# Kernel optimization log

Hardware: AMD Instinct MI355X
Metric: run time of the kernel (lower is better)

The kernel has to match this reference:

```python
import jax, jax.numpy as jnp
import numpy as np

N_EMBD = 256  # scale uses input channel dim C, per original code


def setup_inputs() -> dict:
    key = jax.random.key(0)
    k1, k2, k3, k4 = jax.random.split(key, 4)
    B, T, C, H = 512, 256, 256, 64
    x = jax.random.normal(k1, (B, T, C), dtype=jnp.float32)
    Wq = jax.random.normal(k2, (C, H), dtype=jnp.float32) * (C ** -0.5)
    Wk = jax.random.normal(k3, (C, H), dtype=jnp.float32) * (C ** -0.5)
    Wv = jax.random.normal(k4, (C, H), dtype=jnp.float32) * (C ** -0.5)
    return {"x": x, "Wq": Wq, "Wk": Wk, "Wv": Wv}


def reference(x, Wq, Wk, Wv):
    B, T, C = x.shape
    q = jnp.einsum("btc,ch->bth", x, Wq)  # [B,T,H]
    k = jnp.einsum("btc,ch->bth", x, Wk)
    v = jnp.einsum("btc,ch->bth", x, Wv)
    # Note: original scales by C**-0.5 (input dim), not head_size**-0.5.
    scores = jnp.einsum("bqh,bkh->bqk", q, k) * (C ** -0.5)  # [B,T,T]
    causal = jnp.tril(jnp.ones((T, T), dtype=bool))
    scores = jnp.where(causal, scores, -jnp.inf)
    weights = jax.nn.softmax(scores, axis=-1)
    # Dropout is identity at inference (Keras default training=False).
    out = jnp.einsum("bqk,bkh->bqh", weights, v)  # [B,T,H]
    return out
```

## Files before the change

### kernel.cpp

```cpp
#include <hip/hip_runtime.h>

#define B_  512
#define T_  256
#define C_  256
#define H_  64
#define BT_ (B_ * T_)

typedef unsigned short u16;
typedef __attribute__((ext_vector_type(8))) __bf16 bf16x8;
typedef __attribute__((ext_vector_type(8))) u16 u16x8;
typedef __attribute__((ext_vector_type(4))) float f32x4;

__device__ __forceinline__ u16 f2bf(float f) {
  union { float f; unsigned u; } v; v.f = f;
  unsigned r = v.u + 0x7fffu + ((v.u >> 16) & 1u);
  return (u16)(r >> 16);
}

__device__ __forceinline__ f32x4 mfma16(bf16x8 a, bf16x8 b, f32x4 c) {
  return __builtin_amdgcn_mfma_f32_16x16x32_bf16(a, b, c, 0, 0, 0);
}

__global__ __launch_bounds__(256) void wconv_kernel(
    const float* __restrict__ Wq, const float* __restrict__ Wk,
    const float* __restrict__ Wv, u16* __restrict__ wt) {
  int idx = blockIdx.x * 256 + threadIdx.x;
  int w   = idx >> 14;
  int rem = idx & 16383;
  int h   = rem >> 8;
  int c   = rem & 255;
  const float* W = (w == 0) ? Wq : (w == 1) ? Wk : Wv;
  wt[idx] = f2bf(W[c * H_ + h]);
}

__global__ __launch_bounds__(256) void qkv_kernel(
    const float* __restrict__ x, const u16* __restrict__ wt,
    u16* __restrict__ qo, u16* __restrict__ ko, u16* __restrict__ vto) {
  __shared__ u16 sB[2][192 * 32];

  const int tid  = threadIdx.x;
  const int wave = tid >> 6, lane = tid & 63;
  const int lr = lane & 15, lg = lane >> 4;
  const int row0 = blockIdx.x * 128;

  const f32x4 fzero = {0.f, 0.f, 0.f, 0.f};
  f32x4 acc[2][12];
#pragma unroll
  for (int mt = 0; mt < 2; ++mt)
#pragma unroll
    for (int nt = 0; nt < 12; ++nt) acc[mt][nt] = fzero;

  const float* xp0 = x + (size_t)(row0 + wave * 32 + lr) * C_ + lg * 8;
  const float* xp1 = xp0 + 16 * C_;

  float4 aA[2][2][2];
  u16x8  breg[2][3];

#define LOAD_A(buf, kk)                                     \
  {                                                         \
    aA[buf][0][0] = *(const float4*)(xp0 + (kk) * 32);      \
    aA[buf][0][1] = *(const float4*)(xp0 + (kk) * 32 + 4);  \
    aA[buf][1][0] = *(const float4*)(xp1 + (kk) * 32);      \
    aA[buf][1][1] = *(const float4*)(xp1 + (kk) * 32 + 4);  \
  }

#define LOAD_B(buf, kk)                                                        \
  {                                                                            \
    _Pragma("unroll") for (int i = 0; i < 3; ++i) {                            \
      int d = i * 256 + tid;                                                   \
      breg[buf][i] = *(const u16x8*)(wt + (d >> 2) * C_ + (kk) * 32 + (d & 3) * 8); \
    }                                                                          \
  }

#define WRITE_B(buf)                                        \
  {                                                         \
    _Pragma("unroll") for (int i = 0; i < 3; ++i) {         \
      int d = i * 256 + tid;                                \
      *(u16x8*)&sB[buf][d * 8] = breg[buf][i];              \
    }                                                       \
  }

#define COMPUTE(buf)                                                       \
  {                                                                        \
    bf16x8 af[2];                                                          \
    _Pragma("unroll") for (int mt = 0; mt < 2; ++mt) {                     \
      u16x8 au;                                                            \
      au[0] = f2bf(aA[buf][mt][0].x); au[1] = f2bf(aA[buf][mt][0].y);      \
      au[2] = f2bf(aA[buf][mt][0].z); au[3] = f2bf(aA[buf][mt][0].w);      \
      au[4] = f2bf(aA[buf][mt][1].x); au[5] = f2bf(aA[buf][mt][1].y);      \
      au[6] = f2bf(aA[buf][mt][1].z); au[7] = f2bf(aA[buf][mt][1].w);      \
      af[mt] = __builtin_bit_cast(bf16x8, au);                             \
    }                                                                      \
    _Pragma("unroll") for (int nt = 0; nt < 12; ++nt) {                    \
      bf16x8 bf = *(const bf16x8*)&sB[buf][(nt * 16 + lr) * 32 + lg * 8];  \
      acc[0][nt] = mfma16(af[0], bf, acc[0][nt]);                          \
      acc[1][nt] = mfma16(af[1], bf, acc[1][nt]);                          \
    }                                                                      \
  }

  LOAD_A(0, 0);
  LOAD_B(0, 0);
  WRITE_B(0);
  __syncthreads();

#pragma unroll
  for (int t = 0; t < 8; ++t) {
    const int cur = t & 1, nxt = cur ^ 1;
    if (t < 7) {
      LOAD_A(nxt, t + 1);
      LOAD_B(nxt, t + 1);
    }
    COMPUTE(cur);
    if (t < 7) WRITE_B(nxt);
    __syncthreads();
  }

  const int rbase = row0 + wave * 32 + lg * 4;
#pragma unroll
  for (int nt = 0; nt < 12; ++nt) {
    const int wsel = nt >> 2;
    const int h = (nt & 3) * 16 + lr;
#pragma unroll
    for (int mt = 0; mt < 2; ++mt) {
#pragma unroll
      for (int i = 0; i < 4; ++i) {
        const int r = rbase + mt * 16 + i;
        u16 val = f2bf(acc[mt][nt][i]);
        if (wsel == 0) {
          qo[r * H_ + h] = val;
        } else if (wsel == 1) {
          ko[r * H_ + h] = val;
        } else {
          int bb = r >> 8, tt = r & 255;
          vto[(bb * H_ + h) * T_ + tt] = val;
        }
      }
    }
  }
#undef LOAD_A
#undef LOAD_B
#undef WRITE_B
#undef COMPUTE
}

__global__ __launch_bounds__(256) void attn_kernel(
    const u16* __restrict__ q, const u16* __restrict__ k,
    const u16* __restrict__ vt, float* __restrict__ out) {
  __shared__ u16 sK[256 * 72];
  __shared__ u16 sVt[64 * 264];
  __shared__ u16 sP[4 * 32 * 72];

  const int b = blockIdx.x;
  const int tid = threadIdx.x;

  const u16* kb = k + b * (T_ * H_);
  for (int c = tid; c < 2048; c += 256) {
    int r = c >> 3, off = (c & 7) * 8;
    *(u16x8*)&sK[r * 72 + off] = *(const u16x8*)(kb + c * 8);
  }
  const u16* vb = vt + b * (H_ * T_);
  for (int c = tid; c < 2048; c += 256) {
    int r = c >> 5, off = (c & 31) * 8;
    *(u16x8*)&sVt[r * 264 + off] = *(const u16x8*)(vb + c * 8);
  }
  __syncthreads();

  const int wave = tid >> 6, lane = tid & 63;
  const int lr = lane & 15, lg = lane >> 4;
  u16* sPw = sP + wave * 32 * 72;
  const u16* qb = q + b * (T_ * H_);
  float* ob = out + b * (T_ * H_);

  const f32x4 fzero = {0.f, 0.f, 0.f, 0.f};

#pragma unroll
  for (int ch = 0; ch < 2; ++ch) {
    const int chunk = (ch == 0) ? wave : (7 - wave);
    const int r0 = 32 * chunk;
    const int tl = (r0 + 31) >> 6;

    bf16x8 qf[2][2];
#pragma unroll
    for (int mt = 0; mt < 2; ++mt)
#pragma unroll
      for (int ks = 0; ks < 2; ++ks)
        qf[mt][ks] = *(const bf16x8*)(qb + (r0 + mt * 16 + lr) * H_ + ks * 32 + lg * 8);

    f32x4 o[2][4];
#pragma unroll
    for (int mt = 0; mt < 2; ++mt)
#pragma unroll
      for (int ht = 0; ht < 4; ++ht) o[mt][ht] = fzero;
    float mrow[2][4], lrow[2][4];
#pragma unroll
    for (int mt = 0; mt < 2; ++mt)
#pragma unroll
      for (int i = 0; i < 4; ++i) { mrow[mt][i] = -1e30f; lrow[mt][i] = 0.f; }

    for (int t = 0; t <= tl; ++t) {
      f32x4 s[2][4];
#pragma unroll
      for (int mt = 0; mt < 2; ++mt)
#pragma unroll
        for (int nt = 0; nt < 4; ++nt) s[mt][nt] = fzero;
#pragma unroll
      for (int ks = 0; ks < 2; ++ks) {
#pragma unroll
        for (int nt = 0; nt < 4; ++nt) {
          bf16x8 kf = *(const bf16x8*)&sK[(t * 64 + nt * 16 + lr) * 72 + ks * 32 + lg * 8];
          s[0][nt] = mfma16(qf[0][ks], kf, s[0][nt]);
          s[1][nt] = mfma16(qf[1][ks], kf, s[1][nt]);
        }
      }

      const bool diag = (t == tl);
#pragma unroll
      for (int mt = 0; mt < 2; ++mt) {
#pragma unroll
        for (int i = 0; i < 4; ++i) {
          const int r = r0 + mt * 16 + lg * 4 + i;
          float pv[4];
          float mx = -1e30f;
#pragma unroll
          for (int nt = 0; nt < 4; ++nt) {
            float v = s[mt][nt][i] * 0.0625f;
            if (diag && (t * 64 + nt * 16 + lr > r)) v = -1e30f;
            pv[nt] = v;
            mx = fmaxf(mx, v);
          }
          mx = fmaxf(mx, __shfl_xor(mx, 1));
          mx = fmaxf(mx, __shfl_xor(mx, 2));
          mx = fmaxf(mx, __shfl_xor(mx, 4));
          mx = fmaxf(mx, __shfl_xor(mx, 8));
          float mnew = fmaxf(mrow[mt][i], mx);
          float alpha = __expf(mrow[mt][i] - mnew);
          mrow[mt][i] = mnew;
          float rs = 0.f;
#pragma unroll
          for (int nt = 0; nt < 4; ++nt) {
            float p = __expf(pv[nt] - mnew);
            rs += p;
            sPw[(mt * 16 + lg * 4 + i) * 72 + nt * 16 + lr] = f2bf(p);
          }
          rs += __shfl_xor(rs, 1);
          rs += __shfl_xor(rs, 2);
          rs += __shfl_xor(rs, 4);
          rs += __shfl_xor(rs, 8);
          lrow[mt][i] = lrow[mt][i] * alpha + rs;
#pragma unroll
          for (int ht = 0; ht < 4; ++ht) o[mt][ht][i] *= alpha;
        }
      }

      __builtin_amdgcn_wave_barrier();

#pragma unroll
      for (int ks2 = 0; ks2 < 2; ++ks2) {
        bf16x8 pf0 = *(const bf16x8*)&sPw[(0 + lr) * 72 + ks2 * 32 + lg * 8];
        bf16x8 pf1 = *(const bf16x8*)&sPw[(16 + lr) * 72 + ks2 * 32 + lg * 8];
#pragma unroll
        for (int ht = 0; ht < 4; ++ht) {
          bf16x8 vf = *(const bf16x8*)&sVt[(ht * 16 + lr) * 264 + t * 64 + ks2 * 32 + lg * 8];
          o[0][ht] = mfma16(pf0, vf, o[0][ht]);
          o[1][ht] = mfma16(pf1, vf, o[1][ht]);
        }
      }
      __builtin_amdgcn_wave_barrier();
    }

#pragma unroll
    for (int mt = 0; mt < 2; ++mt) {
#pragma unroll
      for (int i = 0; i < 4; ++i) {
        const float inv = 1.f / lrow[mt][i];
        const int r = r0 + mt * 16 + lg * 4 + i;
#pragma unroll
        for (int ht = 0; ht < 4; ++ht) {
          ob[r * H_ + ht * 16 + lr] = o[mt][ht][i] * inv;
        }
      }
    }
  }
}

extern "C" void kernel_launch(void* const* d_in, const int* in_sizes, int n_in,
                              void* d_out, int out_size, void* d_ws, size_t ws_size,
                              hipStream_t stream) {
  const float* x  = (const float*)d_in[0];
  const float* Wq = (const float*)d_in[1];
  const float* Wk = (const float*)d_in[2];
  const float* Wv = (const float*)d_in[3];
  float* out = (float*)d_out;

  u16* ws = (u16*)d_ws;
  u16* wt = ws;
  u16* qb = ws + 49152;
  u16* kb = qb + (size_t)BT_ * H_;
  u16* vb = kb + (size_t)BT_ * H_;

  wconv_kernel<<<192, 256, 0, stream>>>(Wq, Wk, Wv, wt);
  qkv_kernel<<<BT_ / 128, 256, 0, stream>>>(x, wt, qb, kb, vb);
  attn_kernel<<<B_, 256, 0, stream>>>(qb, kb, vb, out);
}
```

Measured before the change: 262.6 us.

## Split attention per batch across two blocks and read K/V directly from global

The attention kernel now launches two blocks per batch, each wave handling 16-row query chunks paired for causal load balance, instead of one block with 32-row chunks. K and V^T are no longer staged in shared memory. They are loaded from global/L2 straight into registers inside the loop, which shrinks LDS use to the small P buffer, and the kernel adds launch bounds for higher occupancy. The trade-off is that K and V are re-read from cache by every wave instead of once per block, and each K fragment now feeds half as many MFMAs.

```diff
diff --git a/kernel.cpp b/kernel.cpp
--- a/kernel.cpp
+++ b/kernel.cpp
@@ -143,142 +143,118 @@
 #undef COMPUTE
 }
 
-__global__ __launch_bounds__(256) void attn_kernel(
+__global__ __launch_bounds__(256, 4) void attn_kernel(
     const u16* __restrict__ q, const u16* __restrict__ k,
     const u16* __restrict__ vt, float* __restrict__ out) {
-  __shared__ u16 sK[256 * 72];
-  __shared__ u16 sVt[64 * 264];
-  __shared__ u16 sP[4 * 32 * 72];
-
-  const int b = blockIdx.x;
-  const int tid = threadIdx.x;
-
+  __shared__ u16 sP[4 * 16 * 76];
+
+  const int b    = blockIdx.x >> 1;
+  const int half = blockIdx.x & 1;
+  const int wave = threadIdx.x >> 6, lane = threadIdx.x & 63;
+  const int lr = lane & 15, lg = lane >> 4;
+  u16* sPw = sP + wave * 16 * 76;
+
+  const u16* qb = q + b * (T_ * H_);
   const u16* kb = k + b * (T_ * H_);
-  for (int c = tid; c < 2048; c += 256) {
-    int r = c >> 3, off = (c & 7) * 8;
-    *(u16x8*)&sK[r * 72 + off] = *(const u16x8*)(kb + c * 8);
-  }
   const u16* vb = vt + b * (H_ * T_);
-  for (int c = tid; c < 2048; c += 256) {
-    int r = c >> 5, off = (c & 31) * 8;
-    *(u16x8*)&sVt[r * 264 + off] = *(const u16x8*)(vb + c * 8);
-  }
-  __syncthreads();
-
-  const int wave = tid >> 6, lane = tid & 63;
-  const int lr = lane & 15, lg = lane >> 4;
-  u16* sPw = sP + wave * 32 * 72;
-  const u16* qb = q + b * (T_ * H_);
   float* ob = out + b * (T_ * H_);
 
+  const int c0 = half * 4 + wave;
   const f32x4 fzero = {0.f, 0.f, 0.f, 0.f};
 
 #pragma unroll
   for (int ch = 0; ch < 2; ++ch) {
-    const int chunk = (ch == 0) ? wave : (7 - wave);
-    const int r0 = 32 * chunk;
-    const int tl = (r0 + 31) >> 6;
-
-    bf16x8 qf[2][2];
-#pragma unroll
-    for (int mt = 0; mt < 2; ++mt)
-#pragma unroll
-      for (int ks = 0; ks < 2; ++ks)
-        qf[mt][ks] = *(const bf16x8*)(qb + (r0 + mt * 16 + lr) * H_ + ks * 32 + lg * 8);
-
-    f32x4 o[2][4];
-#pragma unroll
-    for (int mt = 0; mt < 2; ++mt)
-#pragma unroll
-      for (int ht = 0; ht < 4; ++ht) o[mt][ht] = fzero;
-    float mrow[2][4], lrow[2][4];
-#pragma unroll
-    for (int mt = 0; mt < 2; ++mt)
-#pragma unroll
-      for (int i = 0; i < 4; ++i) { mrow[mt][i] = -1e30f; lrow[mt][i] = 0.f; }
+    const int c  = ch ? (15 - c0) : c0;
+    const int r0 = c * 16;
+    const int tl = c >> 2;
+
+    bf16x8 qf[2];
+#pragma unroll
+    for (int ks = 0; ks < 2; ++ks)
+      qf[ks] = *(const bf16x8*)(qb + (r0 + lr) * H_ + ks * 32 + lg * 8);
+
+    f32x4 o[4];
+#pragma unroll
+    for (int ht = 0; ht < 4; ++ht) o[ht] = fzero;
+    float mrow[4], lrow[4];
+#pragma unroll
+    for (int i = 0; i < 4; ++i) { mrow[i] = -1e30f; lrow[i] = 0.f; }
 
     for (int t = 0; t <= tl; ++t) {
-      f32x4 s[2][4];
-#pragma unroll
-      for (int mt = 0; mt < 2; ++mt)
-#pragma unroll
-        for (int nt = 0; nt < 4; ++nt) s[mt][nt] = fzero;
+      f32x4 s[4];
+#pragma unroll
+      for (int nt = 0; nt < 4; ++nt) s[nt] = fzero;
 #pragma unroll
       for (int ks = 0; ks < 2; ++ks) {
 #pragma unroll
         for (int nt = 0; nt < 4; ++nt) {
-          bf16x8 kf = *(const bf16x8*)&sK[(t * 64 + nt * 16 + lr) * 72 + ks * 32 + lg * 8];
-          s[0][nt] = mfma16(qf[0][ks], kf, s[0][nt]);
-          s[1][nt] = mfma16(qf[1][ks], kf, s[1][nt]);
-        }
-      }
+          bf16x8 kf = *(const bf16x8*)(kb + (t * 64 + nt * 16 + lr) * H_ + ks * 32 + lg * 8);
+          s[nt] = mfma16(qf[ks], kf, s[nt]);
+        }
+      }
+
+      bf16x8 vreg[2][4];
+#pragma unroll
+      for (int ks2 = 0; ks2 < 2; ++ks2)
+#pragma unroll
+        for (int ht = 0; ht < 4; ++ht)
+          vreg[ks2][ht] = *(const bf16x8*)(vb + (ht * 16 + lr) * T_ + t * 64 + ks2 * 32 + lg * 8);
 
       const bool diag = (t == tl);
 #pragma unroll
-      for (int mt = 0; mt < 2; ++mt) {
-#pragma unroll
-        for (int i = 0; i < 4; ++i) {
-          const int r = r0 + mt * 16 + lg * 4 + i;
-          float pv[4];
-          float mx = -1e30f;
-#pragma unroll
-          for (int nt = 0; nt < 4; ++nt) {
-            float v = s[mt][nt][i] * 0.0625f;
-            if (diag && (t * 64 + nt * 16 + lr > r)) v = -1e30f;
-            pv[nt] = v;
-            mx = fmaxf(mx, v);
-          }
-          mx = fmaxf(mx, __shfl_xor(mx, 1));
-          mx = fmaxf(mx, __shfl_xor(mx, 2));
-          mx = fmaxf(mx, __shfl_xor(mx, 4));
-          mx = fmaxf(mx, __shfl_xor(mx, 8));
-          float mnew = fmaxf(mrow[mt][i], mx);
-          float alpha = __expf(mrow[mt][i] - mnew);
-          mrow[mt][i] = mnew;
-          float rs = 0.f;
-#pragma unroll
-          for (int nt = 0; nt < 4; ++nt) {
-            float p = __expf(pv[nt] - mnew);
-            rs += p;
-            sPw[(mt * 16 + lg * 4 + i) * 72 + nt * 16 + lr] = f2bf(p);
-          }
-          rs += __shfl_xor(rs, 1);
-          rs += __shfl_xor(rs, 2);
-          rs += __shfl_xor(rs, 4);
-          rs += __shfl_xor(rs, 8);
-          lrow[mt][i] = lrow[mt][i] * alpha + rs;
-#pragma unroll
-          for (int ht = 0; ht < 4; ++ht) o[mt][ht][i] *= alpha;
-        }
+      for (int i = 0; i < 4; ++i) {
+        const int r = r0 + lg * 4 + i;
+        float pv[4];
+        float mx = -1e30f;
+#pragma unroll
+        for (int nt = 0; nt < 4; ++nt) {
+          float v = s[nt][i] * 0.0625f;
+          if (diag && (t * 64 + nt * 16 + lr > r)) v = -1e30f;
+          pv[nt] = v;
+          mx = fmaxf(mx, v);
+        }
+        mx = fmaxf(mx, __shfl_xor(mx, 1));
+        mx = fmaxf(mx, __shfl_xor(mx, 2));
+        mx = fmaxf(mx, __shfl_xor(mx, 4));
+        mx = fmaxf(mx, __shfl_xor(mx, 8));
+        float mnew = fmaxf(mrow[i], mx);
+        float alpha = __expf(mrow[i] - mnew);
+        mrow[i] = mnew;
+        float rs = 0.f;
+#pragma unroll
+        for (int nt = 0; nt < 4; ++nt) {
+          float p = __expf(pv[nt] - mnew);
+          rs += p;
+          sPw[(lg * 4 + i) * 76 + nt * 16 + lr] = f2bf(p);
+        }
+        rs += __shfl_xor(rs, 1);
+        rs += __shfl_xor(rs, 2);
+        rs += __shfl_xor(rs, 4);
+        rs += __shfl_xor(rs, 8);
+        lrow[i] = lrow[i] * alpha + rs;
+#pragma unroll
+        for (int ht = 0; ht < 4; ++ht) o[ht][i] *= alpha;
       }
 
       __builtin_amdgcn_wave_barrier();
 
 #pragma unroll
       for (int ks2 = 0; ks2 < 2; ++ks2) {
-        bf16x8 pf0 = *(const bf16x8*)&sPw[(0 + lr) * 72 + ks2 * 32 + lg * 8];
-        bf16x8 pf1 = *(const bf16x8*)&sPw[(16 + lr) * 72 + ks2 * 32 + lg * 8];
-#pragma unroll
-        for (int ht = 0; ht < 4; ++ht) {
-          bf16x8 vf = *(const bf16x8*)&sVt[(ht * 16 + lr) * 264 + t * 64 + ks2 * 32 + lg * 8];
-          o[0][ht] = mfma16(pf0, vf, o[0][ht]);
-          o[1][ht] = mfma16(pf1, vf, o[1][ht]);
-        }
+        bf16x8 pf = *(const bf16x8*)&sPw[lr * 76 + ks2 * 32 + lg * 8];
+#pragma unroll
+        for (int ht = 0; ht < 4; ++ht)
+          o[ht] = mfma16(pf, vreg[ks2][ht], o[ht]);
       }
       __builtin_amdgcn_wave_barrier();
     }
 
 #pragma unroll
-    for (int mt = 0; mt < 2; ++mt) {
-#pragma unroll
-      for (int i = 0; i < 4; ++i) {
-        const float inv = 1.f / lrow[mt][i];
-        const int r = r0 + mt * 16 + lg * 4 + i;
-#pragma unroll
-        for (int ht = 0; ht < 4; ++ht) {
-          ob[r * H_ + ht * 16 + lr] = o[mt][ht][i] * inv;
-        }
-      }
+    for (int i = 0; i < 4; ++i) {
+      const float inv = 1.f / lrow[i];
+      const int r = r0 + lg * 4 + i;
+#pragma unroll
+      for (int ht = 0; ht < 4; ++ht)
+        ob[r * H_ + ht * 16 + lr] = o[ht][i] * inv;
     }
   }
 }
@@ -300,5 +276,5 @@
 
   wconv_kernel<<<192, 256, 0, stream>>>(Wq, Wk, Wv, wt);
   qkv_kernel<<<BT_ / 128, 256, 0, stream>>>(x, wt, qb, kb, vb);
-  attn_kernel<<<B_, 256, 0, stream>>>(qb, kb, vb, out);
-}
+  attn_kernel<<<B_ * 2, 256, 0, stream>>>(qb, kb, vb, out);
+}
```

After: 270.6 us. 1.03x slower.
